# Kernel optimization log

Hardware: AMD Instinct MI355X
Metric: run time of the kernel (lower is better)

Reference implementation:

```python
import jax, jax.numpy as jnp
import numpy as np

B, G, SMAX, H, PH = 16384, 128, 64, 10, 100
# ragged per-gene SNP counts (cycles 4..64), matching gene_input_dims
GENE_DIMS = np.tile(np.array([4, 8, 12, 16, 24, 32, 48, 64], dtype=np.int64), 16)


def setup_inputs() -> dict:
    key = jax.random.key(0)
    ks = jax.random.split(key, 9)
    # mask[g, s] = 1 iff SNP slot s is a real SNP of gene g (ragged -> padded)
    snp_mask = (jnp.arange(SMAX)[None, :] < jnp.asarray(GENE_DIMS)[:, None]).astype(jnp.float32)  # [G, SMAX]
    x = jax.random.normal(ks[0], (B, G, SMAX), dtype=jnp.float32) * snp_mask[None]  # padded SNPs are 0
    # per-gene MLP params: m_i -> H -> 1 ; padded input rows of W1 zeroed (equivalent to ragged Linear)
    W1 = jax.random.normal(ks[1], (G, SMAX, H), dtype=jnp.float32) * 0.1 * snp_mask[:, :, None]
    b1 = jax.random.normal(ks[2], (G, H), dtype=jnp.float32) * 0.1
    W2 = jax.random.normal(ks[3], (G, H), dtype=jnp.float32) * 0.1  # H -> 1, squeezed
    b2 = jax.random.normal(ks[4], (G,), dtype=jnp.float32) * 0.1
    # predictor: G -> PH -> 1
    Wp1 = jax.random.normal(ks[5], (G, PH), dtype=jnp.float32) * 0.1
    bp1 = jax.random.normal(ks[6], (PH,), dtype=jnp.float32) * 0.1
    Wp2 = jax.random.normal(ks[7], (PH, 1), dtype=jnp.float32) * 0.1
    bp2 = jax.random.normal(ks[8], (1,), dtype=jnp.float32) * 0.1
    return {"x": x, "W1": W1, "b1": b1, "W2": W2, "b2": b2,
            "Wp1": Wp1, "bp1": bp1, "Wp2": Wp2, "bp2": bp2}


def reference(x, W1, b1, W2, b2, Wp1, bp1, Wp2, bp2):
    # grouped per-gene MLP: [B,G,SMAX] x [G,SMAX,H] -> [B,G,H]
    h = jax.nn.relu(jnp.einsum('bgs,gsh->bgh', x, W1) + b1[None])
    # per-gene H -> 1 projection, concat over genes -> [B, G]
    gene_layer = jnp.einsum('bgh,gh->bg', h, W2) + b2[None]
    # phenotype predictor: G -> PH -> 1
    p = jax.nn.relu(gene_layer @ Wp1 + bp1)
    return p @ Wp2 + bp2  # [B, 1]
```

## Files before the change

kernel.cpp:

```cpp
#include <hip/hip_runtime.h>

#define B    16384
#define G    128
#define SMAX 64
#define H    10
#define PH   100

__global__ __launch_bounds__(256) void gene_kernel(
    const float* __restrict__ x,  const float* __restrict__ W1,
    const float* __restrict__ b1, const float* __restrict__ W2,
    const float* __restrict__ b2, float* __restrict__ glT)
{
    const int tid = threadIdx.x;
    const int g   = blockIdx.y;
    const int b   = blockIdx.x * 256 + tid;

    const float4* xr = (const float4*)(x + ((size_t)b * G + g) * SMAX);
    float4 xv[16];
    #pragma unroll
    for (int i = 0; i < 16; i++) xv[i] = xr[i];

    const float* __restrict__ w1g = W1 + (size_t)g * SMAX * H;

    float acc[H];
    #pragma unroll
    for (int j = 0; j < H; j++) acc[j] = b1[g * H + j];

    #pragma unroll
    for (int s = 0; s < SMAX; s++) {
        const float xs = ((const float*)xv)[s];
        #pragma unroll
        for (int j = 0; j < H; j++) {
            acc[j] = fmaf(xs, w1g[s * H + j], acc[j]);
        }
    }

    float gene = b2[g];
    #pragma unroll
    for (int j = 0; j < H; j++) {
        gene += fmaxf(acc[j], 0.f) * W2[g * H + j];
    }

    glT[(size_t)g * B + b] = gene;
}

__global__ __launch_bounds__(128) void pred_kernel(
    const float* __restrict__ glT, const float* __restrict__ Wp1,
    const float* __restrict__ bp1, const float* __restrict__ Wp2,
    const float* __restrict__ bp2, float* __restrict__ out)
{
    __shared__ float sgl[8 * G];
    __shared__ float sred[2][8];

    const int tid = threadIdx.x;
    const int b0  = blockIdx.x * 8;

    {
        const float4* gp = (const float4*)(glT + (size_t)tid * B + b0);
        const float4 v0 = gp[0], v1 = gp[1];
        sgl[0 * G + tid] = v0.x; sgl[1 * G + tid] = v0.y;
        sgl[2 * G + tid] = v0.z; sgl[3 * G + tid] = v0.w;
        sgl[4 * G + tid] = v1.x; sgl[5 * G + tid] = v1.y;
        sgl[6 * G + tid] = v1.z; sgl[7 * G + tid] = v1.w;
    }

    const bool  jv   = (tid < PH);
    const float bpj  = jv ? bp1[tid] : 0.f;
    const float wp2j = jv ? Wp2[tid] : 0.f;
    __syncthreads();

    float acc[8];
    #pragma unroll
    for (int b = 0; b < 8; b++) acc[b] = bpj;

    const float2* sgl2 = (const float2*)sgl;
    #pragma unroll
    for (int gc = 0; gc < 4; gc++) {
        float2 w[16];
        #pragma unroll
        for (int p = 0; p < 16; p++) {
            const int gg = gc * 32 + 2 * p;
            w[p].x = jv ? Wp1[(size_t)gg * PH + tid]       : 0.f;
            w[p].y = jv ? Wp1[(size_t)(gg + 1) * PH + tid] : 0.f;
        }
        #pragma unroll
        for (int b = 0; b < 8; b++) {
            float a = acc[b];
            #pragma unroll
            for (int p = 0; p < 16; p++) {
                const float2 s2 = sgl2[b * (G / 2) + gc * 16 + p];
                a = fmaf(w[p].x, s2.x, a);
                a = fmaf(w[p].y, s2.y, a);
            }
            acc[b] = a;
        }
    }

    const int lane = tid & 63;
    const int wv   = tid >> 6;
    #pragma unroll
    for (int b = 0; b < 8; b++) {
        float v = fmaxf(acc[b], 0.f) * wp2j;
        #pragma unroll
        for (int off = 32; off > 0; off >>= 1) v += __shfl_down(v, off, 64);
        if (lane == 0) sred[wv][b] = v;
    }
    __syncthreads();
    if (tid < 8) out[b0 + tid] = sred[0][tid] + sred[1][tid] + bp2[0];
}

extern "C" void kernel_launch(void* const* d_in, const int* in_sizes, int n_in,
                              void* d_out, int out_size, void* d_ws, size_t ws_size,
                              hipStream_t stream) {
    const float* x   = (const float*)d_in[0];
    const float* W1  = (const float*)d_in[1];
    const float* b1  = (const float*)d_in[2];
    const float* W2  = (const float*)d_in[3];
    const float* b2  = (const float*)d_in[4];
    const float* Wp1 = (const float*)d_in[5];
    const float* bp1 = (const float*)d_in[6];
    const float* Wp2 = (const float*)d_in[7];
    const float* bp2 = (const float*)d_in[8];
    float* out = (float*)d_out;
    float* glT = (float*)d_ws;

    gene_kernel<<<dim3(B / 256, G), 256, 0, stream>>>(x, W1, b1, W2, b2, glT);
    pred_kernel<<<dim3(B / 8), 128, 0, stream>>>(glT, Wp1, bp1, Wp2, bp2, out);
}
```

Before: 956.2 us.

## Stage gene-kernel x rows into LDS via async global_load_lds with swizzle

Replaces per-thread strided float4 loads of each 256-byte x row with cooperative global_load_lds transfers, where 16 threads share each row so the global accesses coalesce. The data lands in a 64KB shared tile with an XOR swizzle so the per-thread row reads avoid LDS bank conflicts. The cost is 64KB of LDS per block, which limits occupancy, plus a block-wide barrier before compute.

```diff
diff --git a/kernel.cpp b/kernel.cpp
--- a/kernel.cpp
+++ b/kernel.cpp
@@ -1,4 +1,5 @@
 #include <hip/hip_runtime.h>
+#include <stdint.h>
 
 #define B    16384
 #define G    128
@@ -11,14 +12,28 @@
     const float* __restrict__ b1, const float* __restrict__ W2,
     const float* __restrict__ b2, float* __restrict__ glT)
 {
+    __shared__ float sX[256][SMAX];
+
     const int tid = threadIdx.x;
     const int g   = blockIdx.y;
-    const int b   = blockIdx.x * 256 + tid;
+    const int b0  = blockIdx.x * 256;
 
-    const float4* xr = (const float4*)(x + ((size_t)b * G + g) * SMAX);
-    float4 xv[16];
+    const int sub  = tid >> 4;
+    const int col  = tid & 15;
+    const int csrc = col ^ (sub & 7);
+
+    const float* gbase = x + ((size_t)(b0 + sub) * G + g) * SMAX + csrc * 4;
+    char* lbase = (char*)&sX[0][0] + tid * 16;
+
     #pragma unroll
-    for (int i = 0; i < 16; i++) xv[i] = xr[i];
+    for (int k = 0; k < 16; k++) {
+        __builtin_amdgcn_global_load_lds(
+            (const __attribute__((address_space(1))) uint32_t*)
+                (gbase + (size_t)k * 16 * G * SMAX),
+            (__attribute__((address_space(3))) uint32_t*)(lbase + k * 4096),
+            16, 0, 0);
+    }
+    __syncthreads();
 
     const float* __restrict__ w1g = W1 + (size_t)g * SMAX * H;
 
@@ -26,12 +41,20 @@
     #pragma unroll
     for (int j = 0; j < H; j++) acc[j] = b1[g * H + j];
 
+    const int rsw = tid & 7;
     #pragma unroll
-    for (int s = 0; s < SMAX; s++) {
-        const float xs = ((const float*)xv)[s];
+    for (int i = 0; i < 16; i++) {
+        const int p = i ^ rsw;
+        const float4 xv = *(const float4*)&sX[tid][p * 4];
+        const float xs0 = xv.x, xs1 = xv.y, xs2 = xv.z, xs3 = xv.w;
         #pragma unroll
         for (int j = 0; j < H; j++) {
-            acc[j] = fmaf(xs, w1g[s * H + j], acc[j]);
+            float a = acc[j];
+            a = fmaf(xs0, w1g[(i * 4 + 0) * H + j], a);
+            a = fmaf(xs1, w1g[(i * 4 + 1) * H + j], a);
+            a = fmaf(xs2, w1g[(i * 4 + 2) * H + j], a);
+            a = fmaf(xs3, w1g[(i * 4 + 3) * H + j], a);
+            acc[j] = a;
         }
     }
 
@@ -41,7 +64,7 @@
         gene += fmaxf(acc[j], 0.f) * W2[g * H + j];
     }
 
-    glT[(size_t)g * B + b] = gene;
+    glT[(size_t)g * B + b0 + tid] = gene;
 }
 
 __global__ __launch_bounds__(128) void pred_kernel(
```

Result: slower. 1.024 ms (+7.1%).
